# Optimization experiments

Measured on AMD Instinct MI355X. Metric: run time of the kernel, lower is better.

Reference implementation:

```python
import jax, jax.numpy as jnp
import numpy as np


def conv2d(x, w, b):
    # x: (B,C,H,W), w: (O,I,kh,kw), SAME padding, stride 1
    y = jax.lax.conv_general_dilated(x, w, (1, 1), 'SAME',
                                     dimension_numbers=('NCHW', 'OIHW', 'NCHW'))
    return y + b[None, :, None, None]


def setup_inputs() -> dict:
    key = jax.random.key(0)
    ks = jax.random.split(key, 8)
    B, T, C, H, W = 16, 16, 64, 32, 32
    hd = 64  # hidden_dim == input_dim (required by the module's zero-init of h)

    def winit(k, shape):
        fan_in = shape[1] * shape[2] * shape[3]
        return jax.random.normal(k, shape, jnp.float32) / np.float32(np.sqrt(fan_in))

    return {
        'input_tensor': jax.random.normal(ks[0], (B, T, C, H, W), jnp.float32),
        'time_steps': jnp.arange(T, dtype=jnp.float32),
        'mask': jnp.ones((B, T), jnp.float32),
        # ConvGRUCell params
        'w_gates': winit(ks[1], (2 * hd, C + hd, 3, 3)),
        'b_gates': jnp.zeros((2 * hd,), jnp.float32),
        'w_can': winit(ks[2], (hd, C + hd, 3, 3)),
        'b_can': jnp.zeros((hd,), jnp.float32),
        # ODE func params (tanh(conv3x3(x)))
        'w_ode': winit(ks[3], (hd, hd, 3, 3)),
        'b_ode': jnp.zeros((hd,), jnp.float32),
        # transform_z0: conv1x1 -> ReLU -> conv1x1 (z -> 2z)
        'w_t1': winit(ks[4], (hd, hd, 1, 1)),
        'b_t1': jnp.zeros((hd,), jnp.float32),
        'w_t2': winit(ks[5], (2 * hd, hd, 1, 1)),
        'b_t2': jnp.zeros((2 * hd,), jnp.float32),
    }


def reference(input_tensor, time_steps, mask, w_gates, b_gates, w_can, b_can,
              w_ode, b_ode, w_t1, b_t1, w_t2, b_t2):
    B, T, C, H, W = input_tensor.shape
    hd = w_can.shape[0]

    # run_backwards=True: process i = T-1, T-2, ..., 0
    xs = jnp.flip(input_tensor, axis=1).transpose(1, 0, 2, 3, 4)  # (T,B,C,H,W)
    ms = jnp.flip(mask, axis=1).T                                  # (T,B)
    ts_rev = jnp.flip(time_steps)
    # dt_0 = t_last - (t_last + 0.01) = -0.01 ; dt_k = ts[T-k-1] - ts[T-k]
    dts = jnp.concatenate([jnp.full((1,), -0.01, jnp.float32),
                           ts_rev[1:] - ts_rev[:-1]])               # (T,)

    def step(h, inp):
        x, m, dt = inp
        # Euler ODE step: h_ode = h + ode_func(t, h) * dt
        h_ode = h + jnp.tanh(conv2d(h, w_ode, b_ode)) * dt
        # ConvGRU cell
        comb = jnp.concatenate([x, h_ode], axis=1)
        gates = jax.nn.sigmoid(conv2d(comb, w_gates, b_gates))
        reset, update = gates[:, :hd], gates[:, hd:]
        cand = jnp.tanh(conv2d(jnp.concatenate([x, reset * h_ode], axis=1),
                               w_can, b_can))
        h_new = (1.0 - update) * h_ode + update * cand
        mm = m[:, None, None, None]
        h_next = mm * h_new + (1.0 - mm) * h_ode
        return h_next, None

    h0 = jnp.zeros((B, hd, H, W), input_tensor.dtype)
    last_yi, _ = jax.lax.scan(step, h0, (xs, ms, dts))

    z = jax.nn.relu(conv2d(last_yi, w_t1, b_t1))
    z = conv2d(z, w_t2, b_t2)
    mean_z0 = z[:, :hd]
    std_z0 = jnp.abs(z[:, hd:])
    return mean_z0, std_z0
```

## Files before the change

### kernel.cpp

```cpp
#include <hip/hip_runtime.h>
#include <hip/hip_bf16.h>

#define BB 16
#define TT 16

typedef short short8  __attribute__((ext_vector_type(8)));
typedef short short4v __attribute__((ext_vector_type(4)));
typedef float f32x4   __attribute__((ext_vector_type(4)));

__device__ __forceinline__ ushort f2bf(float f) {
    uint u = __float_as_uint(f);
    u += 0x7FFFu + ((u >> 16) & 1u);
    return (ushort)(u >> 16);
}
__device__ __forceinline__ float bf2f(ushort h) { return __uint_as_float(((uint)h) << 16); }
__device__ __forceinline__ float fast_sigmoid(float x) { return 1.0f / (1.0f + __expf(-x)); }
__device__ __forceinline__ float fast_tanh(float x) {
    float e = __expf(2.0f * x);
    return 1.0f - 2.0f / (e + 1.0f);
}
__device__ __forceinline__ short8 pack8(const float4 a, const float4 b) {
    short8 r;
    r[0]=(short)f2bf(a.x); r[1]=(short)f2bf(a.y); r[2]=(short)f2bf(a.z); r[3]=(short)f2bf(a.w);
    r[4]=(short)f2bf(b.x); r[5]=(short)f2bf(b.y); r[6]=(short)f2bf(b.z); r[7]=(short)f2bf(b.w);
    return r;
}

__global__ __launch_bounds__(256)
void pack_frag(const float* __restrict__ src, ushort* __restrict__ dst,
               int CO, int CIN, int NT) {
    int KC = CIN >> 5, CBn = CO >> 4;
    int total = NT * CBn * KC * 64;
    for (int i = blockIdx.x * 256 + threadIdx.x; i < total; i += gridDim.x * 256) {
        int lane = i & 63, rest = i >> 6;
        int kc = rest % KC;
        int rest2 = rest / KC;
        int cb = rest2 % CBn, tap = rest2 / CBn;
        int co = cb * 16 + (lane & 15);
        int ci0 = kc * 32 + (lane >> 4) * 8;
        short8 v;
        #pragma unroll
        for (int e = 0; e < 8; ++e)
            v[e] = (short)f2bf(src[((size_t)co * CIN + ci0 + e) * NT + tap]);
        *(short8*)(dst + (size_t)i * 8) = v;
    }
}

__global__ __launch_bounds__(256)
void x_transpose(const float* __restrict__ src, ushort* __restrict__ dst) {
    __shared__ float tile[64 * 256];
    const int bt = blockIdx.x, q = blockIdx.y, tid = threadIdx.x;
    const float* s = src + (size_t)bt * 64 * 1024 + q * 256;
    for (int i = tid; i < 64 * 256; i += 256)
        tile[i] = s[(size_t)(i >> 8) * 1024 + (i & 255)];
    __syncthreads();
    const int p = q * 256 + tid;
    ushort* d = dst + ((size_t)bt * 1026 + 1 + p) * 64;
    #pragma unroll
    for (int c8 = 0; c8 < 8; ++c8) {
        short8 v;
        #pragma unroll
        for (int e = 0; e < 8; ++e) v[e] = (short)f2bf(tile[(c8 * 8 + e) * 256 + tid]);
        *(short8*)(d + ((c8 ^ (p & 7)) << 3)) = v;
    }
    if (q == 0 && tid < 8)
        *(short8*)(dst + (size_t)bt * 1026 * 64 + tid * 8) = (short8)0;
    if (q == 3 && tid < 8)
        *(short8*)(dst + ((size_t)bt * 1026 + 1025) * 64 + tid * 8) = (short8)0;
}

__global__ __launch_bounds__(512, 1)
void fused_step(const ushort* __restrict__ x_cl,
                const float* __restrict__ h_in,
                const ushort* __restrict__ h_inb,
                float* __restrict__ h_out,
                ushort* __restrict__ h_outb,
                const ushort* __restrict__ wfO,
                const ushort* __restrict__ wfG,
                const ushort* __restrict__ wfC,
                const float* __restrict__ b_ode,
                const float* __restrict__ b_gates,
                const float* __restrict__ b_can,
                const float* __restrict__ tsteps,
                const float* __restrict__ mask,
                int t)
{
    extern __shared__ ushort smem[];
    float*  smemf = (float*)smem;
    ushort* hbuf  = smem;
    ushort* xbuf  = smem + 17408;
    ushort* obuf  = smem + 30464;
    ushort* rhbuf = smem;
    float*  ubuf  = smemf + 4352;
    float*  hode  = smemf + 21760;

    const int rt = blockIdx.x, b = blockIdx.y;
    const int R  = rt * 2;
    const int tid = threadIdx.x;
    const int w = tid >> 6, lane = tid & 63, lr = lane & 15, lg = lane >> 4;

    const ushort* xbb = x_cl + ((size_t)(b * TT + (TT - 1 - t))) * 1026 * 64;
    const ushort* hbb = h_inb + (size_t)b * 1026 * 64;
    const float*  hb  = h_in  + (size_t)b * 65536;

    for (int i = tid; i < 2176; i += 512) {
        const int tr = i / 272, rem = i - tr * 272;
        const int hc = rem >> 3;
        const int y  = R - 3 + tr;
        short8 v = (short8)0;
        if ((unsigned)y < 32u && hc != 0 && hc != 33)
            v = *(const short8*)(hbb + ((size_t)(y * 32 + hc)) * 64 + (rem & 7) * 8);
        *(short8*)(hbuf + (size_t)i * 8) = v;
    }
    for (int i = tid; i < 1632; i += 512) {
        const int tr = i / 272, rem = i - tr * 272;
        const int hc = rem >> 3;
        const int y  = R - 2 + tr;
        short8 v = (short8)0;
        if ((unsigned)y < 32u && hc != 0 && hc != 33)
            v = *(const short8*)(xbb + ((size_t)(y * 32 + hc)) * 64 + (rem & 7) * 8);
        *(short8*)(xbuf + (size_t)i * 8) = v;
    }
    for (int i = tid; i < 1632; i += 512) {
        const int tr = i / 272, rem = i - tr * 272;
        const int hc = rem >> 3;
        const int y  = R - 2 + tr;
        if (hc == 0 || hc == 33 || (unsigned)y >= 32u)
            *(short8*)(obuf + (size_t)i * 8) = (short8)0;
    }
    __syncthreads();

    {
        const int cb0 = (w & 1) * 2;
        const int pxg = w >> 1;
        f32x4 accA[2][3];
        #pragma unroll
        for (int i = 0; i < 2; ++i)
            #pragma unroll
            for (int j = 0; j < 3; ++j) accA[i][j] = 0;

        #pragma unroll
        for (int tap = 0; tap < 9; ++tap) {
            const int ky = tap / 3, kx = tap - ky * 3;
            #pragma unroll
            for (int kc = 0; kc < 2; ++kc) {
                short8 a0 = *(const short8*)(wfO + (size_t)(((tap * 4 + cb0 + 0) * 2 + kc) * 512) + lane * 8);
                short8 a1 = *(const short8*)(wfO + (size_t)(((tap * 4 + cb0 + 1) * 2 + kc) * 512) + lane * 8);
                #pragma unroll
                for (int j = 0; j < 3; ++j) {
                    const int p  = (3 * pxg + j) * 16 + lr;
                    const int tr = (p >> 5) + ky, hc = (p & 31) + kx;
                    short8 bf = *(const short8*)(hbuf + (tr * 34 + hc) * 64 + ((((kc << 2) + lg) ^ ((hc + 7) & 7)) << 3));
                    accA[0][j] = __builtin_amdgcn_mfma_f32_16x16x32_bf16(a0, bf, accA[0][j], 0, 0, 0);
                    accA[1][j] = __builtin_amdgcn_mfma_f32_16x16x32_bf16(a1, bf, accA[1][j], 0, 0, 0);
                }
            }
        }
        const float dt = (t == 0) ? -0.01f : (tsteps[TT - 1 - t] - tsteps[TT - t]);
        #pragma unroll
        for (int i = 0; i < 2; ++i) {
            #pragma unroll
            for (int j = 0; j < 3; ++j) {
                const int co0 = (cb0 + i) * 16 + lg * 4;
                const int p = (3 * pxg + j) * 16 + lr;
                const int orow = p >> 5, c = p & 31;
                const int y = R - 2 + orow;
                if ((unsigned)y < 32u) {
                    const f32x4 h4 = *(const f32x4*)(hb + ((size_t)(y * 32 + c)) * 64 + co0);
                    const f32x4 b4 = *(const f32x4*)(b_ode + co0);
                    f32x4 ho;
                    #pragma unroll
                    for (int r = 0; r < 4; ++r)
                        ho[r] = h4[r] + fast_tanh(accA[i][j][r] + b4[r]) * dt;
                    short4v s;
                    #pragma unroll
                    for (int r = 0; r < 4; ++r) s[r] = (short)f2bf(ho[r]);
                    *(short4v*)(obuf + (orow * 34 + c + 1) * 64 + (((co0 >> 3) ^ (c & 7)) << 3) + (co0 & 7)) = s;
                    if ((unsigned)(y - R) < 2u)
                        *(f32x4*)(hode + ((y - R) * 32 + c) * 64 + (((co0 >> 2) ^ (c & 15)) << 2)) = ho;
                }
            }
        }
    }
    __syncthreads();

    for (int i = tid; i < 1088; i += 512) {
        const int tr = i / 272, rem = i - tr * 272;
        const int hc = rem >> 3;
        const int y  = R - 1 + tr;
        if (hc == 0 || hc == 33 || (unsigned)y >= 32u)
            *(short8*)(rhbuf + (size_t)i * 8) = (short8)0;
    }

    {
        const int cq = w & 3, ph = w >> 2;
        f32x4 accB[2][4];
        #pragma unroll
        for (int i = 0; i < 2; ++i)
            #pragma unroll
            for (int j = 0; j < 4; ++j) accB[i][j] = 0;

        #pragma unroll
        for (int tap = 0; tap < 9; ++tap) {
            const int ky = tap / 3, kx = tap - ky * 3;
            #pragma unroll
            for (int kc = 0; kc < 4; ++kc) {
                const ushort* reg = (kc < 2) ? xbuf : obuf;
                short8 a0 = *(const short8*)(wfG + (size_t)(((tap * 8 + 2 * cq + 0) * 4 + kc) * 512) + lane * 8);
                short8 a1 = *(const short8*)(wfG + (size_t)(((tap * 8 + 2 * cq + 1) * 4 + kc) * 512) + lane * 8);
                #pragma unroll
                for (int j = 0; j < 4; ++j) {
                    const int f  = 4 * ph + j;
                    const int tr = (f >> 1) + ky;
                    const int hc = (f & 1) * 16 + lr + kx;
                    short8 bf = *(const short8*)(reg + (tr * 34 + hc) * 64 + (((((kc & 1) << 2) + lg) ^ ((hc + 7) & 7)) << 3));
                    accB[0][j] = __builtin_amdgcn_mfma_f32_16x16x32_bf16(a0, bf, accB[0][j], 0, 0, 0);
                    accB[1][j] = __builtin_amdgcn_mfma_f32_16x16x32_bf16(a1, bf, accB[1][j], 0, 0, 0);
                }
            }
        }
        #pragma unroll
        for (int i = 0; i < 2; ++i) {
            const int cog = (2 * cq + i) * 16 + lg * 4;
            const f32x4 b4 = *(const f32x4*)(b_gates + cog);
            #pragma unroll
            for (int j = 0; j < 4; ++j) {
                const int f = 4 * ph + j;
                const int y = R - 1 + (f >> 1);
                const int c = (f & 1) * 16 + lr;
                if (cq < 2) {
                    if ((unsigned)y < 32u) {
                        const int tro = (f >> 1) + 1;
                        const int key = (((cog >> 3) ^ (c & 7)) << 3) + (cog & 7);
                        short4v ho4 = *(const short4v*)(obuf + (tro * 34 + c + 1) * 64 + key);
                        short4v s;
                        #pragma unroll
                        for (int r = 0; r < 4; ++r)
                            s[r] = (short)f2bf(fast_sigmoid(accB[i][j][r] + b4[r]) * bf2f((ushort)ho4[r]));
                        *(short4v*)(rhbuf + ((f >> 1) * 34 + c + 1) * 64 + key) = s;
                    }
                } else if ((unsigned)(y - R) < 2u) {
                    const int cu = cog - 64;
                    f32x4 u;
                    #pragma unroll
                    for (int r = 0; r < 4; ++r)
                        u[r] = fast_sigmoid(accB[i][j][r] + b4[r]);
                    *(f32x4*)(ubuf + ((y - R) * 32 + c) * 64 + (((cu >> 2) ^ (c & 15)) << 2)) = u;
                }
            }
        }
    }
    __syncthreads();

    {
        const int cf = w & 3, ph2 = w >> 2;
        f32x4 accC[2];
        accC[0] = 0; accC[1] = 0;

        #pragma unroll
        for (int tap = 0; tap < 9; ++tap) {
            const int ky = tap / 3, kx = tap - ky * 3;
            #pragma unroll
            for (int kc = 0; kc < 4; ++kc) {
                const ushort* reg = (kc < 2) ? xbuf : rhbuf;
                const int rowoff = (kc < 2) ? 1 : 0;
                short8 a = *(const short8*)(wfC + (size_t)(((tap * 4 + cf) * 4 + kc) * 512) + lane * 8);
                #pragma unroll
                for (int j = 0; j < 2; ++j) {
                    const int tr = ph2 + rowoff + ky;
                    const int hc = j * 16 + lr + kx;
                    short8 bf = *(const short8*)(reg + (tr * 34 + hc) * 64 + (((((kc & 1) << 2) + lg) ^ ((hc + 7) & 7)) << 3));
                    accC[j] = __builtin_amdgcn_mfma_f32_16x16x32_bf16(a, bf, accC[j], 0, 0, 0);
                }
            }
        }
        const float m = mask[b * TT + (TT - 1 - t)];
        const int y = R + ph2;
        const int co0 = cf * 16 + lg * 4;
        const f32x4 b4 = *(const f32x4*)(b_can + co0);
        #pragma unroll
        for (int j = 0; j < 2; ++j) {
            const int c = j * 16 + lr;
            const int pi = ph2 * 32 + c;
            const int sw = ((co0 >> 2) ^ (c & 15)) << 2;
            const f32x4 ho = *(const f32x4*)(hode + pi * 64 + sw);
            const f32x4 u  = *(const f32x4*)(ubuf + pi * 64 + sw);
            f32x4 o;
            short4v s;
            #pragma unroll
            for (int r = 0; r < 4; ++r) {
                const float cand = fast_tanh(accC[j][r] + b4[r]);
                o[r] = ho[r] + m * u[r] * (cand - ho[r]);
                s[r] = (short)f2bf(o[r]);
            }
            const int pix = y * 32 + c;
            *(f32x4*)(h_out + (size_t)b * 65536 + (size_t)pix * 64 + co0) = o;
            *(short4v*)(h_outb + ((size_t)b * 1026 + 1 + pix) * 64
                        + (((co0 >> 3) ^ (c & 7)) << 3) + (co0 & 7)) = s;
        }
    }
}

__global__ __launch_bounds__(256)
void head_mfma(const float* __restrict__ h,
               const ushort* __restrict__ w1f, const float* __restrict__ b1,
               const ushort* __restrict__ w2f, const float* __restrict__ b2,
               float* __restrict__ outp)
{
    __shared__ ushort hlds[64 * 64];
    __shared__ ushort zlds[64 * 64];
    const int blk = blockIdx.x, b = blk >> 4, pixb = (blk & 15) * 64;
    const int tid = threadIdx.x, wv = tid >> 6, lane = tid & 63, lr = lane & 15, lg = lane >> 4;
    const float* hb = h + ((size_t)b * 1024 + pixb) * 64;

    for (int idx = tid; idx < 64 * 8; idx += 256) {
        const int c = idx & 7, px = idx >> 3;
        const float4* p = (const float4*)(hb + (size_t)px * 64 + c * 8);
        *(short8*)(hlds + px * 64 + ((c ^ (px & 7)) << 3)) = pack8(p[0], p[1]);
    }
    __syncthreads();

    f32x4 acc1[4]; acc1[0]=0; acc1[1]=0; acc1[2]=0; acc1[3]=0;
    #pragma unroll
    for (int kc = 0; kc < 2; ++kc) {
        short8 a = *(const short8*)(w1f + (((size_t)wv * 2 + kc) * 64 + lane) * 8);
        #pragma unroll
        for (int p = 0; p < 4; ++p) {
            const int hp = p * 16 + lr;
            short8 bf = *(const short8*)(hlds + hp * 64 + (((kc * 4 + lg) ^ (hp & 7)) << 3));
            acc1[p] = __builtin_amdgcn_mfma_f32_16x16x32_bf16(a, bf, acc1[p], 0, 0, 0);
        }
    }
    {
        const int co0 = wv * 16 + lg * 4;
        const f32x4 b4 = *(const f32x4*)(b1 + co0);
        #pragma unroll
        for (int p = 0; p < 4; ++p) {
            const int px = p * 16 + lr;
            short4v s;
            #pragma unroll
            for (int r = 0; r < 4; ++r)
                s[r] = (short)f2bf(fmaxf(acc1[p][r] + b4[r], 0.0f));
            *(short4v*)(zlds + px * 64 + (((co0 >> 3) ^ (px & 7)) << 3) + (co0 & 7)) = s;
        }
    }
    __syncthreads();

    f32x4 acc2[2][4];
    #pragma unroll
    for (int gi = 0; gi < 2; ++gi)
        #pragma unroll
        for (int p = 0; p < 4; ++p) acc2[gi][p] = 0;
    #pragma unroll
    for (int kc = 0; kc < 2; ++kc) {
        short8 a0 = *(const short8*)(w2f + ((((size_t)wv * 2 + 0) * 2 + kc) * 64 + lane) * 8);
        short8 a1 = *(const short8*)(w2f + ((((size_t)wv * 2 + 1) * 2 + kc) * 64 + lane) * 8);
        #pragma unroll
        for (int p = 0; p < 4; ++p) {
            const int hp = p * 16 + lr;
            short8 bf = *(const short8*)(zlds + hp * 64 + (((kc * 4 + lg) ^ (hp & 7)) << 3));
            acc2[0][p] = __builtin_amdgcn_mfma_f32_16x16x32_bf16(a0, bf, acc2[0][p], 0, 0, 0);
            acc2[1][p] = __builtin_amdgcn_mfma_f32_16x16x32_bf16(a1, bf, acc2[1][p], 0, 0, 0);
        }
    }
    #pragma unroll
    for (int gi = 0; gi < 2; ++gi) {
        const int co0 = wv * 32 + gi * 16 + lg * 4;
        const f32x4 b4 = *(const f32x4*)(b2 + co0);
        #pragma unroll
        for (int p = 0; p < 4; ++p) {
            const int px = pixb + p * 16 + lr;
            #pragma unroll
            for (int r = 0; r < 4; ++r) {
                const int co = co0 + r;
                const float v = acc2[gi][p][r] + b4[r];
                if (co < 64)
                    outp[((size_t)b * 64 + co) * 1024 + px] = v;
                else
                    outp[(size_t)BB * 64 * 1024 + ((size_t)b * 64 + (co - 64)) * 1024 + px] = fabsf(v);
            }
        }
    }
}

extern "C" void kernel_launch(void* const* d_in, const int* in_sizes, int n_in,
                              void* d_out, int out_size, void* d_ws, size_t ws_size,
                              hipStream_t stream)
{
    const float* xall    = (const float*)d_in[0];
    const float* tsteps  = (const float*)d_in[1];
    const float* mask    = (const float*)d_in[2];
    const float* w_gates = (const float*)d_in[3];
    const float* b_gates = (const float*)d_in[4];
    const float* w_can   = (const float*)d_in[5];
    const float* b_can   = (const float*)d_in[6];
    const float* w_ode   = (const float*)d_in[7];
    const float* b_ode   = (const float*)d_in[8];
    const float* w_t1    = (const float*)d_in[9];
    const float* b_t1    = (const float*)d_in[10];
    const float* w_t2    = (const float*)d_in[11];
    const float* b_t2    = (const float*)d_in[12];
    float* out = (float*)d_out;

    float*  h0   = (float*)d_ws;
    float*  h1   = h0 + (size_t)BB * 65536;
    ushort* h0b  = (ushort*)(h1 + (size_t)BB * 65536);
    ushort* h1b  = h0b + (size_t)BB * 1026 * 64;
    ushort* x_cl = h1b + (size_t)BB * 1026 * 64;
    ushort* wfG  = x_cl + (size_t)BB * TT * 1026 * 64;
    ushort* wfC  = wfG + (size_t)9 * 8 * 4 * 512;
    ushort* wfO  = wfC + (size_t)9 * 4 * 4 * 512;
    ushort* wf1  = wfO + (size_t)9 * 4 * 2 * 512;
    ushort* wf2  = wf1 + (size_t)4 * 2 * 512;

    hipMemsetAsync(h0, 0, (size_t)BB * 65536 * sizeof(float), stream);
    hipMemsetAsync(h0b, 0, (size_t)BB * 1026 * 64 * 2 * sizeof(ushort), stream);
    x_transpose<<<dim3(256, 4), 256, 0, stream>>>(xall, x_cl);
    pack_frag<<<dim3(72), 256, 0, stream>>>(w_gates, wfG, 128, 128, 9);
    pack_frag<<<dim3(36), 256, 0, stream>>>(w_can,   wfC, 64, 128, 9);
    pack_frag<<<dim3(18), 256, 0, stream>>>(w_ode,   wfO, 64, 64, 9);
    pack_frag<<<dim3(2),  256, 0, stream>>>(w_t1,    wf1, 64, 64, 1);
    pack_frag<<<dim3(4),  256, 0, stream>>>(w_t2,    wf2, 128, 64, 1);

    hipFuncSetAttribute(reinterpret_cast<const void*>(fused_step),
                        hipFuncAttributeMaxDynamicSharedMemorySize, 103424);

    for (int t = 0; t < TT; ++t) {
        const float*  hin   = (t & 1) ? h1  : h0;
        float*        hout  = (t & 1) ? h0  : h1;
        const ushort* hinb  = (t & 1) ? h1b : h0b;
        ushort*       houtb = (t & 1) ? h0b : h1b;
        fused_step<<<dim3(16, BB), 512, 103424, stream>>>(x_cl, hin, hinb, hout, houtb,
                                                          wfO, wfG, wfC,
                                                          b_ode, b_gates, b_can,
                                                          tsteps, mask, t);
    }
    head_mfma<<<dim3(256), 256, 0, stream>>>(h0, wf1, b_t1, wf2, b_t2, out);
}
```

Measured before the change: 482.5 us.

## Precompute input-dependent conv contributions for all timesteps in one parallel kernel

```diff
diff --git a/kernel.cpp b/kernel.cpp
--- a/kernel.cpp
+++ b/kernel.cpp
@@ -28,59 +28,112 @@
 
 __global__ __launch_bounds__(256)
 void pack_frag(const float* __restrict__ src, ushort* __restrict__ dst,
-               int CO, int CIN, int NT) {
-    int KC = CIN >> 5, CBn = CO >> 4;
-    int total = NT * CBn * KC * 64;
+               int CO, int CINfull, int ci_base, int KCp, int cb_base, int CBT, int NT) {
+    int CBn = CO >> 4;
+    int total = NT * CBn * KCp * 64;
     for (int i = blockIdx.x * 256 + threadIdx.x; i < total; i += gridDim.x * 256) {
         int lane = i & 63, rest = i >> 6;
-        int kc = rest % KC;
-        int rest2 = rest / KC;
+        int kc = rest % KCp;
+        int rest2 = rest / KCp;
         int cb = rest2 % CBn, tap = rest2 / CBn;
         int co = cb * 16 + (lane & 15);
-        int ci0 = kc * 32 + (lane >> 4) * 8;
+        int ci0 = ci_base + kc * 32 + (lane >> 4) * 8;
         short8 v;
         #pragma unroll
         for (int e = 0; e < 8; ++e)
-            v[e] = (short)f2bf(src[((size_t)co * CIN + ci0 + e) * NT + tap]);
-        *(short8*)(dst + (size_t)i * 8) = v;
-    }
-}
-
-__global__ __launch_bounds__(256)
-void x_transpose(const float* __restrict__ src, ushort* __restrict__ dst) {
-    __shared__ float tile[64 * 256];
-    const int bt = blockIdx.x, q = blockIdx.y, tid = threadIdx.x;
-    const float* s = src + (size_t)bt * 64 * 1024 + q * 256;
-    for (int i = tid; i < 64 * 256; i += 256)
-        tile[i] = s[(size_t)(i >> 8) * 1024 + (i & 255)];
+            v[e] = (short)f2bf(src[((size_t)co * CINfull + ci0 + e) * NT + tap]);
+        size_t fi = ((size_t)(tap * CBT + cb_base + cb)) * KCp + kc;
+        *(short8*)(dst + (fi * 64 + lane) * 8) = v;
+    }
+}
+
+__global__ __launch_bounds__(512)
+void conv_x192(const float* __restrict__ xall,
+               const ushort* __restrict__ wfX,
+               const float* __restrict__ b_gates,
+               const float* __restrict__ b_can,
+               ushort* __restrict__ axc)
+{
+    __shared__ ushort xb[4 * 34 * 64];
+    const int rt = blockIdx.x, bt = blockIdx.y;
+    const int R  = rt * 2;
+    const int tid = threadIdx.x;
+    const float* xs = xall + (size_t)bt * 65536;
+
+    for (int i = tid; i < 4 * 34 * 32; i += 512) {
+        const int hp = i >> 5, cp = i & 31;
+        const int tr = hp / 34, hc = hp - tr * 34;
+        const int y = R - 1 + tr, x = hc - 1;
+        uint val = 0;
+        if ((unsigned)y < 32u && (unsigned)x < 32u) {
+            const int pix = y * 32 + x;
+            float v0 = xs[(size_t)(cp * 2) * 1024 + pix];
+            float v1 = xs[(size_t)(cp * 2 + 1) * 1024 + pix];
+            val = (uint)f2bf(v0) | ((uint)f2bf(v1) << 16);
+        }
+        const int c = cp >> 2;
+        const int s = c ^ ((hc + 7) & 7);
+        ((uint*)xb)[hp * 32 + (s << 2) + (cp & 3)] = val;
+    }
     __syncthreads();
-    const int p = q * 256 + tid;
-    ushort* d = dst + ((size_t)bt * 1026 + 1 + p) * 64;
-    #pragma unroll
-    for (int c8 = 0; c8 < 8; ++c8) {
-        short8 v;
-        #pragma unroll
-        for (int e = 0; e < 8; ++e) v[e] = (short)f2bf(tile[(c8 * 8 + e) * 256 + tid]);
-        *(short8*)(d + ((c8 ^ (p & 7)) << 3)) = v;
-    }
-    if (q == 0 && tid < 8)
-        *(short8*)(dst + (size_t)bt * 1026 * 64 + tid * 8) = (short8)0;
-    if (q == 3 && tid < 8)
-        *(short8*)(dst + ((size_t)bt * 1026 + 1025) * 64 + tid * 8) = (short8)0;
+
+    const int w = tid >> 6, lane = tid & 63, lr = lane & 15, lg = lane >> 4;
+    const int cb0 = (w & 3) * 3;
+    const int pf0 = (w >> 2) * 2;
+
+    f32x4 acc[3][2];
+    #pragma unroll
+    for (int i = 0; i < 3; ++i) { acc[i][0] = 0; acc[i][1] = 0; }
+
+    #pragma unroll
+    for (int tap = 0; tap < 9; ++tap) {
+        const int ky = tap / 3, kx = tap - ky * 3;
+        #pragma unroll
+        for (int kc = 0; kc < 2; ++kc) {
+            short8 a[3];
+            #pragma unroll
+            for (int i = 0; i < 3; ++i)
+                a[i] = *(const short8*)(wfX + (size_t)(((tap * 12 + cb0 + i) * 2 + kc) * 512) + lane * 8);
+            #pragma unroll
+            for (int j = 0; j < 2; ++j) {
+                const int px = (pf0 + j) * 16 + lr;
+                const int tr = (px >> 5) + ky, hc = (px & 31) + kx;
+                short8 bf = *(const short8*)(xb + (tr * 34 + hc) * 64 + (((kc * 4 + lg) ^ ((hc + 7) & 7)) << 3));
+                #pragma unroll
+                for (int i = 0; i < 3; ++i)
+                    acc[i][j] = __builtin_amdgcn_mfma_f32_16x16x32_bf16(a[i], bf, acc[i][j], 0, 0, 0);
+            }
+        }
+    }
+
+    #pragma unroll
+    for (int i = 0; i < 3; ++i) {
+        const int co0 = (cb0 + i) * 16 + lg * 4;
+        const float* bsrc = (co0 < 128) ? (b_gates + co0) : (b_can + co0 - 128);
+        const f32x4 b4 = *(const f32x4*)bsrc;
+        #pragma unroll
+        for (int j = 0; j < 2; ++j) {
+            const int px = (pf0 + j) * 16 + lr;
+            const int y = R + (px >> 5), xx = px & 31;
+            short4v s;
+            #pragma unroll
+            for (int r = 0; r < 4; ++r)
+                s[r] = (short)f2bf(acc[i][j][r] + b4[r]);
+            *(short4v*)(axc + ((size_t)bt * 1024 + y * 32 + xx) * 192 + co0) = s;
+        }
+    }
 }
 
 __global__ __launch_bounds__(512, 1)
-void fused_step(const ushort* __restrict__ x_cl,
+void fused_step(const ushort* __restrict__ axc,
                 const float* __restrict__ h_in,
                 const ushort* __restrict__ h_inb,
                 float* __restrict__ h_out,
                 ushort* __restrict__ h_outb,
                 const ushort* __restrict__ wfO,
-                const ushort* __restrict__ wfG,
-                const ushort* __restrict__ wfC,
+                const ushort* __restrict__ wfGh,
+                const ushort* __restrict__ wfCh,
                 const float* __restrict__ b_ode,
-                const float* __restrict__ b_gates,
-                const float* __restrict__ b_can,
                 const float* __restrict__ tsteps,
                 const float* __restrict__ mask,
                 int t)
@@ -88,20 +141,20 @@
     extern __shared__ ushort smem[];
     float*  smemf = (float*)smem;
     ushort* hbuf  = smem;
-    ushort* xbuf  = smem + 17408;
-    ushort* obuf  = smem + 30464;
+    ushort* obuf  = smem + 17408;
     ushort* rhbuf = smem;
     float*  ubuf  = smemf + 4352;
-    float*  hode  = smemf + 21760;
+    float*  hode  = smemf + 15232;
 
     const int rt = blockIdx.x, b = blockIdx.y;
     const int R  = rt * 2;
     const int tid = threadIdx.x;
     const int w = tid >> 6, lane = tid & 63, lr = lane & 15, lg = lane >> 4;
-
-    const ushort* xbb = x_cl + ((size_t)(b * TT + (TT - 1 - t))) * 1026 * 64;
+    const int bti = b * TT + (TT - 1 - t);
+
     const ushort* hbb = h_inb + (size_t)b * 1026 * 64;
     const float*  hb  = h_in  + (size_t)b * 65536;
+    const ushort* axb = axc + (size_t)bti * 1024 * 192;
 
     for (int i = tid; i < 2176; i += 512) {
         const int tr = i / 272, rem = i - tr * 272;
@@ -111,15 +164,6 @@
         if ((unsigned)y < 32u && hc != 0 && hc != 33)
             v = *(const short8*)(hbb + ((size_t)(y * 32 + hc)) * 64 + (rem & 7) * 8);
         *(short8*)(hbuf + (size_t)i * 8) = v;
-    }
-    for (int i = tid; i < 1632; i += 512) {
-        const int tr = i / 272, rem = i - tr * 272;
-        const int hc = rem >> 3;
-        const int y  = R - 2 + tr;
-        short8 v = (short8)0;
-        if ((unsigned)y < 32u && hc != 0 && hc != 33)
-            v = *(const short8*)(xbb + ((size_t)(y * 32 + hc)) * 64 + (rem & 7) * 8);
-        *(short8*)(xbuf + (size_t)i * 8) = v;
     }
     for (int i = tid; i < 1632; i += 512) {
         const int tr = i / 272, rem = i - tr * 272;
@@ -196,24 +240,36 @@
         const int cq = w & 3, ph = w >> 2;
         f32x4 accB[2][4];
         #pragma unroll
-        for (int i = 0; i < 2; ++i)
-            #pragma unroll
-            for (int j = 0; j < 4; ++j) accB[i][j] = 0;
+        for (int i = 0; i < 2; ++i) {
+            const int cog0 = (2 * cq + i) * 16 + lg * 4;
+            #pragma unroll
+            for (int j = 0; j < 4; ++j) {
+                const int f = 4 * ph + j;
+                const int y = R - 1 + (f >> 1);
+                const int c = (f & 1) * 16 + lr;
+                f32x4 g = {0.f, 0.f, 0.f, 0.f};
+                if ((unsigned)y < 32u) {
+                    short4v gx = *(const short4v*)(axb + ((size_t)(y * 32 + c)) * 192 + cog0);
+                    #pragma unroll
+                    for (int r = 0; r < 4; ++r) g[r] = bf2f((ushort)gx[r]);
+                }
+                accB[i][j] = g;
+            }
+        }
 
         #pragma unroll
         for (int tap = 0; tap < 9; ++tap) {
             const int ky = tap / 3, kx = tap - ky * 3;
             #pragma unroll
-            for (int kc = 0; kc < 4; ++kc) {
-                const ushort* reg = (kc < 2) ? xbuf : obuf;
-                short8 a0 = *(const short8*)(wfG + (size_t)(((tap * 8 + 2 * cq + 0) * 4 + kc) * 512) + lane * 8);
-                short8 a1 = *(const short8*)(wfG + (size_t)(((tap * 8 + 2 * cq + 1) * 4 + kc) * 512) + lane * 8);
+            for (int kc = 0; kc < 2; ++kc) {
+                short8 a0 = *(const short8*)(wfGh + (size_t)(((tap * 8 + 2 * cq + 0) * 2 + kc) * 512) + lane * 8);
+                short8 a1 = *(const short8*)(wfGh + (size_t)(((tap * 8 + 2 * cq + 1) * 2 + kc) * 512) + lane * 8);
                 #pragma unroll
                 for (int j = 0; j < 4; ++j) {
                     const int f  = 4 * ph + j;
                     const int tr = (f >> 1) + ky;
                     const int hc = (f & 1) * 16 + lr + kx;
-                    short8 bf = *(const short8*)(reg + (tr * 34 + hc) * 64 + (((((kc & 1) << 2) + lg) ^ ((hc + 7) & 7)) << 3));
+                    short8 bf = *(const short8*)(obuf + (tr * 34 + hc) * 64 + ((((kc << 2) + lg) ^ ((hc + 7) & 7)) << 3));
                     accB[0][j] = __builtin_amdgcn_mfma_f32_16x16x32_bf16(a0, bf, accB[0][j], 0, 0, 0);
                     accB[1][j] = __builtin_amdgcn_mfma_f32_16x16x32_bf16(a1, bf, accB[1][j], 0, 0, 0);
                 }
@@ -222,7 +278,6 @@
         #pragma unroll
         for (int i = 0; i < 2; ++i) {
             const int cog = (2 * cq + i) * 16 + lg * 4;
-            const f32x4 b4 = *(const f32x4*)(b_gates + cog);
             #pragma unroll
             for (int j = 0; j < 4; ++j) {
                 const int f = 4 * ph + j;
@@ -236,7 +291,7 @@
                         short4v s;
                         #pragma unroll
                         for (int r = 0; r < 4; ++r)
-                            s[r] = (short)f2bf(fast_sigmoid(accB[i][j][r] + b4[r]) * bf2f((ushort)ho4[r]));
+                            s[r] = (short)f2bf(fast_sigmoid(accB[i][j][r]) * bf2f((ushort)ho4[r]));
                         *(short4v*)(rhbuf + ((f >> 1) * 34 + c + 1) * 64 + key) = s;
                     }
                 } else if ((unsigned)(y - R) < 2u) {
@@ -244,7 +299,7 @@
                     f32x4 u;
                     #pragma unroll
                     for (int r = 0; r < 4; ++r)
-                        u[r] = fast_sigmoid(accB[i][j][r] + b4[r]);
+                        u[r] = fast_sigmoid(accB[i][j][r]);
                     *(f32x4*)(ubuf + ((y - R) * 32 + c) * 64 + (((cu >> 2) ^ (c & 15)) << 2)) = u;
                 }
             }
@@ -254,30 +309,36 @@
 
     {
         const int cf = w & 3, ph2 = w >> 2;
+        const int co0 = cf * 16 + lg * 4;
         f32x4 accC[2];
-        accC[0] = 0; accC[1] = 0;
+        #pragma unroll
+        for (int j = 0; j < 2; ++j) {
+            const int c = j * 16 + lr;
+            const int pix = (R + ph2) * 32 + c;
+            short4v cx = *(const short4v*)(axb + (size_t)pix * 192 + 128 + co0);
+            f32x4 g;
+            #pragma unroll
+            for (int r = 0; r < 4; ++r) g[r] = bf2f((ushort)cx[r]);
+            accC[j] = g;
+        }
 
         #pragma unroll
         for (int tap = 0; tap < 9; ++tap) {
             const int ky = tap / 3, kx = tap - ky * 3;
             #pragma unroll
-            for (int kc = 0; kc < 4; ++kc) {
-                const ushort* reg = (kc < 2) ? xbuf : rhbuf;
-                const int rowoff = (kc < 2) ? 1 : 0;
-                short8 a = *(const short8*)(wfC + (size_t)(((tap * 4 + cf) * 4 + kc) * 512) + lane * 8);
+            for (int kc = 0; kc < 2; ++kc) {
+                short8 a = *(const short8*)(wfCh + (size_t)(((tap * 4 + cf) * 2 + kc) * 512) + lane * 8);
                 #pragma unroll
                 for (int j = 0; j < 2; ++j) {
-                    const int tr = ph2 + rowoff + ky;
+                    const int tr = ph2 + ky;
                     const int hc = j * 16 + lr + kx;
-                    short8 bf = *(const short8*)(reg + (tr * 34 + hc) * 64 + (((((kc & 1) << 2) + lg) ^ ((hc + 7) & 7)) << 3));
+                    short8 bf = *(const short8*)(rhbuf + (tr * 34 + hc) * 64 + ((((kc << 2) + lg) ^ ((hc + 7) & 7)) << 3));
                     accC[j] = __builtin_amdgcn_mfma_f32_16x16x32_bf16(a, bf, accC[j], 0, 0, 0);
                 }
             }
         }
         const float m = mask[b * TT + (TT - 1 - t)];
         const int y = R + ph2;
-        const int co0 = cf * 16 + lg * 4;
-        const f32x4 b4 = *(const f32x4*)(b_can + co0);
         #pragma unroll
         for (int j = 0; j < 2; ++j) {
             const int c = j * 16 + lr;
@@ -289,7 +350,7 @@
             short4v s;
             #pragma unroll
             for (int r = 0; r < 4; ++r) {
-                const float cand = fast_tanh(accC[j][r] + b4[r]);
+                const float cand = fast_tanh(accC[j][r]);
                 o[r] = ho[r] + m * u[r] * (cand - ho[r]);
                 s[r] = (short)f2bf(o[r]);
             }
@@ -406,34 +467,38 @@
     float*  h1   = h0 + (size_t)BB * 65536;
     ushort* h0b  = (ushort*)(h1 + (size_t)BB * 65536);
     ushort* h1b  = h0b + (size_t)BB * 1026 * 64;
-    ushort* x_cl = h1b + (size_t)BB * 1026 * 64;
-    ushort* wfG  = x_cl + (size_t)BB * TT * 1026 * 64;
-    ushort* wfC  = wfG + (size_t)9 * 8 * 4 * 512;
-    ushort* wfO  = wfC + (size_t)9 * 4 * 4 * 512;
-    ushort* wf1  = wfO + (size_t)9 * 4 * 2 * 512;
-    ushort* wf2  = wf1 + (size_t)4 * 2 * 512;
+    ushort* axc  = h1b + (size_t)BB * 1026 * 64;
+    ushort* wfX  = axc + (size_t)256 * 1024 * 192;
+    ushort* wfGh = wfX  + (size_t)216 * 512;
+    ushort* wfCh = wfGh + (size_t)144 * 512;
+    ushort* wfO  = wfCh + (size_t)72 * 512;
+    ushort* wf1  = wfO  + (size_t)72 * 512;
+    ushort* wf2  = wf1  + (size_t)8 * 512;
 
     hipMemsetAsync(h0, 0, (size_t)BB * 65536 * sizeof(float), stream);
     hipMemsetAsync(h0b, 0, (size_t)BB * 1026 * 64 * 2 * sizeof(ushort), stream);
-    x_transpose<<<dim3(256, 4), 256, 0, stream>>>(xall, x_cl);
-    pack_frag<<<dim3(72), 256, 0, stream>>>(w_gates, wfG, 128, 128, 9);
-    pack_frag<<<dim3(36), 256, 0, stream>>>(w_can,   wfC, 64, 128, 9);
-    pack_frag<<<dim3(18), 256, 0, stream>>>(w_ode,   wfO, 64, 64, 9);
-    pack_frag<<<dim3(2),  256, 0, stream>>>(w_t1,    wf1, 64, 64, 1);
-    pack_frag<<<dim3(4),  256, 0, stream>>>(w_t2,    wf2, 128, 64, 1);
+
+    pack_frag<<<dim3(36), 256, 0, stream>>>(w_gates, wfX,  128, 128, 0,  2, 0, 12, 9);
+    pack_frag<<<dim3(18), 256, 0, stream>>>(w_can,   wfX,  64,  128, 0,  2, 8, 12, 9);
+    pack_frag<<<dim3(36), 256, 0, stream>>>(w_gates, wfGh, 128, 128, 64, 2, 0, 8,  9);
+    pack_frag<<<dim3(18), 256, 0, stream>>>(w_can,   wfCh, 64,  128, 64, 2, 0, 4,  9);
+    pack_frag<<<dim3(18), 256, 0, stream>>>(w_ode,   wfO,  64,  64,  0,  2, 0, 4,  9);
+    pack_frag<<<dim3(2),  256, 0, stream>>>(w_t1,    wf1,  64,  64,  0,  2, 0, 4,  1);
+    pack_frag<<<dim3(4),  256, 0, stream>>>(w_t2,    wf2,  128, 64,  0,  2, 0, 8,  1);
+
+    conv_x192<<<dim3(16, 256), 512, 0, stream>>>(xall, wfX, b_gates, b_can, axc);
 
     hipFuncSetAttribute(reinterpret_cast<const void*>(fused_step),
-                        hipFuncAttributeMaxDynamicSharedMemorySize, 103424);
+                        hipFuncAttributeMaxDynamicSharedMemorySize, 77312);
 
     for (int t = 0; t < TT; ++t) {
         const float*  hin   = (t & 1) ? h1  : h0;
         float*        hout  = (t & 1) ? h0  : h1;
         const ushort* hinb  = (t & 1) ? h1b : h0b;
         ushort*       houtb = (t & 1) ? h0b : h1b;
-        fused_step<<<dim3(16, BB), 512, 103424, stream>>>(x_cl, hin, hinb, hout, houtb,
-                                                          wfO, wfG, wfC,
-                                                          b_ode, b_gates, b_can,
-                                                          tsteps, mask, t);
+        fused_step<<<dim3(16, BB), 512, 77312, stream>>>(axc, hin, hinb, hout, houtb,
+                                                         wfO, wfGh, wfCh,
+                                                         b_ode, tsteps, mask, t);
     }
     head_mfma<<<dim3(256), 256, 0, stream>>>(h0, wf1, b_t1, wf2, b_t2, out);
 }
```

After: 526.9 us. +9.2%, slower.
